# Optimization experiments

Hardware: AMD Instinct MI355X
Metric: run time of the kernel (lower is better)

Reference implementation:

```python
import jax, jax.numpy as jnp
import numpy as np

B, NQ, S, D = 8, 1024, 2048, 512

def setup_inputs() -> dict:
    key = jax.random.key(0)
    k1, k2, k3, k4 = jax.random.split(key, 4)
    queries = jax.random.normal(k1, (B, NQ, D), dtype=jnp.float32)
    keys = jax.random.normal(k2, (B, S, D), dtype=jnp.float32)
    values = jax.random.normal(k3, (B, S, D), dtype=jnp.float32)
    mask = jax.random.randint(k4, (B, NQ, S), 0, 2, dtype=jnp.int32)
    return {"queries": queries, "keys": keys, "values": values, "mask": mask}

def reference(queries, keys, values, mask):
    # scores: dot-product attention scores (b, nq, s)
    scores = jnp.einsum('bqd,bsd->bqs', queries, keys)
    attention_dist = jax.nn.softmax(scores, axis=2)
    # mask then renormalize over seq axis
    attention_dist = attention_dist * mask.astype(attention_dist.dtype)
    attention_dist = attention_dist / attention_dist.sum(axis=2, keepdims=True)
    # weighted sum of values: equivalent to (dist.unsqueeze(3) * values.unsqueeze(1)).sum(2)
    final_vector = jnp.einsum('bqs,bsd->bqd', attention_dist, values)
    return final_vector
```

## Files before the change

kernel.cpp:

```cpp
#include <hip/hip_runtime.h>


#define Bz 8
#define NQz 1024
#define Sz 2048
#define Dz 512
#define QTT 128
#define TS 32
#define KP 520
#define PP 40

typedef _Float16 f16x8 __attribute__((ext_vector_type(8)));
typedef float f32x4 __attribute__((ext_vector_type(4)));
typedef unsigned short ushort_t;

#define AS1(p) ((const __attribute__((address_space(1))) unsigned int*)(p))
#define AS3(p) ((__attribute__((address_space(3))) unsigned int*)(p))
#define DRAIN_ALL() __builtin_amdgcn_s_waitcnt(0)

__device__ __forceinline__ ushort_t f2h(float x) {
  _Float16 h = (_Float16)x;
  return __builtin_bit_cast(ushort_t, h);
}
__device__ __forceinline__ float h2f(ushort_t u) {
  return (float)__builtin_bit_cast(_Float16, u);
}

__global__ __launch_bounds__(256)
void prep(const float* __restrict__ K, const float* __restrict__ V,
          const int* __restrict__ Mi, ushort_t* __restrict__ Kf,
          ushort_t* __restrict__ Vt, unsigned* __restrict__ Mp) {
  __shared__ ushort_t sT[64][41];
  const int t = threadIdx.x;
  int bx = blockIdx.x;
  if (bx < 2048) {
    const size_t base = (size_t)bx * 4096 + t * 4;
#pragma unroll
    for (int i = 0; i < 4; ++i) {
      size_t e = base + i * 1024;
      float4 v = *(const float4*)(K + e);
      uint2 w;
      w.x = (unsigned)f2h(v.x) | ((unsigned)f2h(v.y) << 16);
      w.y = (unsigned)f2h(v.z) | ((unsigned)f2h(v.w) << 16);
      *(uint2*)(Kf + e) = w;
    }
    return;
  }
  bx -= 2048;
  if (bx < 4096) {
    const int b = bx >> 9;
    const int rest = bx & 511;
    const int st = rest >> 4;
    const int dt = rest & 15;
    const int s0 = st * 64, d0 = dt * 32;
    const float* Vb = V + ((size_t)b * Sz + s0) * Dz + d0;
#pragma unroll
    for (int i = 0; i < 2; ++i) {
      int idx = t + 256 * i;
      int s = idx >> 3;
      int dc = (idx & 7) * 4;
      float4 v = *(const float4*)(Vb + (size_t)s * Dz + dc);
      uint2 w;
      w.x = (unsigned)f2h(v.x) | ((unsigned)f2h(v.y) << 16);
      w.y = (unsigned)f2h(v.z) | ((unsigned)f2h(v.w) << 16);
      *(uint2*)(&sT[s][dc]) = w;
    }
    __syncthreads();
    ushort_t* VtB = Vt + ((size_t)b * Dz + d0) * Sz + s0;
    int d = t >> 3, c = t & 7;
    uint4 u;
    ushort_t* tp = (ushort_t*)&u;
#pragma unroll
    for (int j = 0; j < 8; ++j) tp[j] = sT[c * 8 + j][d];
    *(uint4*)(VtB + (size_t)d * Sz + c * 8) = u;
    return;
  }
  bx -= 4096;
  const int lane = t & 63;
#pragma unroll
  for (int i = 0; i < 4; ++i) {
    const size_t base = (size_t)bx * 4096 + i * 1024 + t * 4;
    const int4 mv = *(const int4*)(Mi + base);
    unsigned nib = (mv.x ? 1u : 0u) | (mv.y ? 2u : 0u) |
                   (mv.z ? 4u : 0u) | (mv.w ? 8u : 0u);
    unsigned v = nib << ((lane & 7) * 4);
    v |= __shfl_xor(v, 1);
    v |= __shfl_xor(v, 2);
    v |= __shfl_xor(v, 4);
    if ((lane & 7) == 0) Mp[bx * 128 + i * 32 + (t >> 3)] = v;
  }
}

template <int SPLIT>
__global__ __launch_bounds__(512, 2)
void attn_flash(const float* __restrict__ Q, const unsigned* __restrict__ Mp,
                const ushort_t* __restrict__ Kf, const ushort_t* __restrict__ Vt,
                ushort_t* __restrict__ Opart, float* __restrict__ Mpart,
                float* __restrict__ Lpart) {
  __shared__ ushort_t sK[2][TS][KP];
  __shared__ ushort_t sV[2][Dz][TS];
  __shared__ ushort_t sP[8][16][PP];

  const int tid  = threadIdx.x;
  const int wave = tid >> 6;
  const int lane = tid & 63;
  const int l16  = lane & 15;
  const int quad = lane >> 4;

  const int bxr = blockIdx.x;
  const int b   = bxr & 7;
  const int rest = bxr >> 3;
  const int qt  = rest / SPLIT;
  const int sh  = rest % SPLIT;
  const int q0  = qt * QTT;
  const int SLEN = Sz / SPLIT;
  const int NTt  = SLEN / TS;
  const int sbeg = sh * SLEN;
  const int qw   = q0 + wave * 16;

  const float*    Qb  = Q  + ((size_t)b * NQz + qw) * Dz;
  const ushort_t* KfB = Kf + (size_t)b * Sz * Dz;
  const ushort_t* VtB = Vt + (size_t)b * Dz * Sz;
  const unsigned* MpB = Mp + ((size_t)b * NQz + qw) * (Sz / 32);

  const int vql  = (lane & 3) ^ ((lane >> 3) & 3);
  const int vcol = (quad ^ ((l16 >> 1) & 3)) * 8;

  auto issue_tile = [&](int s0n, int bsel) {
#pragma unroll
    for (int j = 0; j < 4; ++j) {
      int row = wave * 4 + j;
      const ushort_t* gp = KfB + (size_t)(s0n + row) * Dz + lane * 8;
      __builtin_amdgcn_global_load_lds(AS1(gp), AS3(&sK[bsel][row][0]), 16, 0, 0);
    }
#pragma unroll
    for (int j = 0; j < 4; ++j) {
      int dbase = wave * 64 + j * 16;
      int d = dbase + (lane >> 2);
      const ushort_t* gp = VtB + (size_t)d * Sz + s0n + vql * 8;
      __builtin_amdgcn_global_load_lds(AS1(gp), AS3(&sV[bsel][dbase][0]), 16, 0, 0);
    }
  };
  auto load_mask = [&](int s0n) -> unsigned {
    return MpB[(size_t)l16 * (Sz / 32) + (s0n >> 5)];
  };

  issue_tile(sbeg, 0);
  unsigned msk_cur = load_mask(sbeg);

  f16x8 qa[16];
  {
    const float* qrow = Qb + (size_t)l16 * Dz;
#pragma unroll
    for (int kk = 0; kk < 16; ++kk) {
      const float4 a = *(const float4*)(qrow + kk * 32 + quad * 8);
      const float4 c = *(const float4*)(qrow + kk * 32 + quad * 8 + 4);
      f16x8 h;
      h[0] = (_Float16)a.x; h[1] = (_Float16)a.y;
      h[2] = (_Float16)a.z; h[3] = (_Float16)a.w;
      h[4] = (_Float16)c.x; h[5] = (_Float16)c.y;
      h[6] = (_Float16)c.z; h[7] = (_Float16)c.w;
      qa[kk] = h;
    }
  }
  if (NTt > 1) issue_tile(sbeg + TS, 1);
  DRAIN_ALL();
  __syncthreads();

  float m_ln = -1e30f, l_ln = 0.0f;
  f32x4 oacc[32];
#pragma unroll
  for (int nt = 0; nt < 32; ++nt) oacc[nt] = (f32x4){0.f, 0.f, 0.f, 0.f};

  const ushort_t* vbase0 = &sV[0][0][0] + (size_t)l16 * TS + vcol;
  const ushort_t* vbase1 = &sV[1][0][0] + (size_t)l16 * TS + vcol;

  for (int i = 0; i < NTt; ++i) {
    const int buf = i & 1;
    if (i) {
      DRAIN_ALL();
      __syncthreads();
      if (i + 1 < NTt) issue_tile(sbeg + (i + 1) * TS, buf ^ 1);
    }
    unsigned msk_nxt = (i + 1 < NTt) ? load_mask(sbeg + (i + 1) * TS) : 0u;

    f32x4 a00 = (f32x4){0.f,0.f,0.f,0.f}, a01 = (f32x4){0.f,0.f,0.f,0.f};
    f32x4 a10 = (f32x4){0.f,0.f,0.f,0.f}, a11 = (f32x4){0.f,0.f,0.f,0.f};
    {
      const ushort_t* kh0 = &sK[buf][l16][quad * 8];
      const ushort_t* kh1 = &sK[buf][16 + l16][quad * 8];
#pragma unroll
      for (int kk = 0; kk < 16; kk += 2) {
        f16x8 k00 = *(const f16x8*)(kh0 + kk * 32);
        f16x8 k10 = *(const f16x8*)(kh1 + kk * 32);
        f16x8 k01 = *(const f16x8*)(kh0 + kk * 32 + 32);
        f16x8 k11 = *(const f16x8*)(kh1 + kk * 32 + 32);
        a00 = __builtin_amdgcn_mfma_f32_16x16x32_f16(k00, qa[kk], a00, 0, 0, 0);
        a10 = __builtin_amdgcn_mfma_f32_16x16x32_f16(k10, qa[kk], a10, 0, 0, 0);
        a01 = __builtin_amdgcn_mfma_f32_16x16x32_f16(k01, qa[kk+1], a01, 0, 0, 0);
        a11 = __builtin_amdgcn_mfma_f32_16x16x32_f16(k11, qa[kk+1], a11, 0, 0, 0);
      }
    }
    f32x4 s0v, s1v;
#pragma unroll
    for (int r = 0; r < 4; ++r) { s0v[r] = a00[r] + a01[r]; s1v[r] = a10[r] + a11[r]; }

    const unsigned mb = msk_cur;
    float se0[4], se1[4];
#pragma unroll
    for (int r = 0; r < 4; ++r) {
      se0[r] = ((mb >> (quad * 4 + r)) & 1u)      ? s0v[r] : -1e30f;
      se1[r] = ((mb >> (16 + quad * 4 + r)) & 1u) ? s1v[r] : -1e30f;
    }
    float rmax = fmaxf(fmaxf(fmaxf(se0[0], se0[1]), fmaxf(se0[2], se0[3])),
                       fmaxf(fmaxf(se1[0], se1[1]), fmaxf(se1[2], se1[3])));
    rmax = fmaxf(rmax, __shfl_xor(rmax, 16));
    rmax = fmaxf(rmax, __shfl_xor(rmax, 32));

    ushort_t pb0[4], pb1[4];
    float rsum = 0.f;
#pragma unroll
    for (int r = 0; r < 4; ++r) {
      float p0 = ((mb >> (quad * 4 + r)) & 1u)      ? __expf(se0[r] - rmax) : 0.f;
      float p1 = ((mb >> (16 + quad * 4 + r)) & 1u) ? __expf(se1[r] - rmax) : 0.f;
      pb0[r] = f2h(p0); pb1[r] = f2h(p1);
      rsum += h2f(pb0[r]) + h2f(pb1[r]);
    }
    {
      uint2 w0, w1;
      w0.x = (unsigned)pb0[0] | ((unsigned)pb0[1] << 16);
      w0.y = (unsigned)pb0[2] | ((unsigned)pb0[3] << 16);
      w1.x = (unsigned)pb1[0] | ((unsigned)pb1[1] << 16);
      w1.y = (unsigned)pb1[2] | ((unsigned)pb1[3] << 16);
      *(uint2*)(&sP[wave][l16][quad * 4]) = w0;
      *(uint2*)(&sP[wave][l16][16 + quad * 4]) = w1;
    }
    rsum += __shfl_xor(rsum, 16);
    rsum += __shfl_xor(rsum, 32);

    float m_new = fmaxf(m_ln, rmax);
    float scl   = __expf(rmax - m_new);
    float al_ln = __expf(m_ln - m_new);
    bool  grw   = m_new > m_ln;
    l_ln = al_ln * l_ln + scl * rsum;
    m_ln = m_new;

    f16x8 praw = *(const f16x8*)(&sP[wave][l16][quad * 8]);
    f16x8 pa;
    {
      _Float16 sh16 = (_Float16)scl;
#pragma unroll
      for (int j = 0; j < 8; ++j) pa[j] = praw[j] * sh16;
    }

    if (__any((int)grw)) {
      float al[4];
#pragma unroll
      for (int r = 0; r < 4; ++r) al[r] = __shfl(al_ln, quad * 4 + r);
#pragma unroll
      for (int nt = 0; nt < 32; ++nt)
#pragma unroll
        for (int r = 0; r < 4; ++r) oacc[nt][r] *= al[r];
    }

    const ushort_t* vb_ = buf ? vbase1 : vbase0;
#pragma unroll
    for (int nt = 0; nt < 32; ++nt) {
      f16x8 vb = *(const f16x8*)(vb_ + nt * 512);
      oacc[nt] = __builtin_amdgcn_mfma_f32_16x16x32_f16(pa, vb, oacc[nt], 0, 0, 0);
    }

    msk_cur = msk_nxt;
  }

  const size_t rbase = (size_t)(b * SPLIT + sh) * NQz + q0 + wave * 16;
#pragma unroll
  for (int nt = 0; nt < 32; ++nt) {
#pragma unroll
    for (int r = 0; r < 4; ++r) {
      Opart[(rbase + quad * 4 + r) * Dz + nt * 16 + l16] = f2h(oacc[nt][r]);
    }
  }
  if (quad == 0) {
    Mpart[rbase + l16] = m_ln;
    Lpart[rbase + l16] = l_ln;
  }
}

template <int SPLIT>
__global__ __launch_bounds__(256)
void combine(const ushort_t* __restrict__ Opart, const float* __restrict__ Mpart,
             const float* __restrict__ Lpart, float* __restrict__ Out) {
  int gid = blockIdx.x * 256 + threadIdx.x;
  int row = gid >> 7;
  int b   = row >> 10;
  int q   = row & 1023;
  int c   = (gid & 127) * 4;
  float mv[SPLIT], lv[SPLIT];
  float m = -1e30f;
#pragma unroll
  for (int p = 0; p < SPLIT; ++p) {
    size_t ip = (size_t)(b * SPLIT + p) * NQz + q;
    mv[p] = Mpart[ip];
    lv[p] = Lpart[ip];
    m = fmaxf(m, mv[p]);
  }
  float w[SPLIT], denom = 0.f;
#pragma unroll
  for (int p = 0; p < SPLIT; ++p) {
    w[p] = __expf(mv[p] - m);
    denom += w[p] * lv[p];
  }
  float inv = 1.0f / denom;
  float4 o = {0.f, 0.f, 0.f, 0.f};
#pragma unroll
  for (int p = 0; p < SPLIT; ++p) {
    size_t ip = (size_t)(b * SPLIT + p) * NQz + q;
    const ushort_t* op = Opart + ip * Dz + c;
    uint2 raw = *(const uint2*)op;
    o.x += w[p] * h2f((ushort_t)(raw.x & 0xffff));
    o.y += w[p] * h2f((ushort_t)(raw.x >> 16));
    o.z += w[p] * h2f((ushort_t)(raw.y & 0xffff));
    o.w += w[p] * h2f((ushort_t)(raw.y >> 16));
  }
  o.x *= inv; o.y *= inv; o.z *= inv; o.w *= inv;
  *(float4*)(Out + ((size_t)b * NQz + q) * Dz + c) = o;
}

extern "C" void kernel_launch(void* const* d_in, const int* in_sizes, int n_in,
                              void* d_out, int out_size, void* d_ws, size_t ws_size,
                              hipStream_t stream) {
  const float* Q = (const float*)d_in[0];
  const float* K = (const float*)d_in[1];
  const float* V = (const float*)d_in[2];
  const int*   M = (const int*)d_in[3];
  float* O = (float*)d_out;

  const size_t NKV   = (size_t)Bz * Sz * Dz;
  const size_t maskW = (size_t)Bz * NQz * (Sz / 32);

  ushort_t* Kf = (ushort_t*)d_ws;
  ushort_t* Vt = Kf + NKV;
  unsigned* Mp = (unsigned*)(Vt + NKV);
  ushort_t* Opart = (ushort_t*)(Mp + maskW);

  auto need_bytes = [&](int S) -> size_t {
    return NKV * 2 * 2 + maskW * 4
         + (size_t)Bz * S * NQz * Dz * 2
         + (size_t)Bz * S * NQz * 4 * 2;
  };

  prep<<<dim3(10240), dim3(256), 0, stream>>>(K, V, M, Kf, Vt, Mp);

  if (ws_size >= need_bytes(4)) {
    constexpr int S = 4;
    float* Mpart = (float*)(Opart + (size_t)Bz * S * NQz * Dz);
    float* Lpart = Mpart + (size_t)Bz * S * NQz;
    attn_flash<S><<<dim3(8 * (NQz / QTT) * S), dim3(512), 0, stream>>>(
        Q, Mp, Kf, Vt, Opart, Mpart, Lpart);
    combine<S><<<dim3(4096), dim3(256), 0, stream>>>(Opart, Mpart, Lpart, O);
  } else {
    constexpr int S = 2;
    float* Mpart = (float*)(Opart + (size_t)Bz * S * NQz * Dz);
    float* Lpart = Mpart + (size_t)Bz * S * NQz;
    attn_flash<S><<<dim3(8 * (NQz / QTT) * S), dim3(512), 0, stream>>>(
        Q, Mp, Kf, Vt, Opart, Mpart, Lpart);
    combine<S><<<dim3(4096), dim3(256), 0, stream>>>(Opart, Mpart, Lpart, O);
  }
}
```

Measured before the change: 246.9 us.

## Partition PV by D columns per wave, load V directly into registers

```diff
diff --git a/kernel.cpp b/kernel.cpp
--- a/kernel.cpp
+++ b/kernel.cpp
@@ -98,8 +98,8 @@
                 ushort_t* __restrict__ Opart, float* __restrict__ Mpart,
                 float* __restrict__ Lpart) {
   __shared__ ushort_t sK[2][TS][KP];
-  __shared__ ushort_t sV[2][Dz][TS];
-  __shared__ ushort_t sP[8][16][PP];
+  __shared__ ushort_t sP[QTT][PP];
+  __shared__ float    sAl[QTT];
 
   const int tid  = threadIdx.x;
   const int wave = tid >> 6;
@@ -123,29 +123,21 @@
   const ushort_t* VtB = Vt + (size_t)b * Dz * Sz;
   const unsigned* MpB = Mp + ((size_t)b * NQz + qw) * (Sz / 32);
 
-  const int vql  = (lane & 3) ^ ((lane >> 3) & 3);
-  const int vcol = (quad ^ ((l16 >> 1) & 3)) * 8;
-
-  auto issue_tile = [&](int s0n, int bsel) {
+  auto issue_k = [&](int s0n, int bsel) {
 #pragma unroll
     for (int j = 0; j < 4; ++j) {
       int row = wave * 4 + j;
       const ushort_t* gp = KfB + (size_t)(s0n + row) * Dz + lane * 8;
       __builtin_amdgcn_global_load_lds(AS1(gp), AS3(&sK[bsel][row][0]), 16, 0, 0);
     }
-#pragma unroll
-    for (int j = 0; j < 4; ++j) {
-      int dbase = wave * 64 + j * 16;
-      int d = dbase + (lane >> 2);
-      const ushort_t* gp = VtB + (size_t)d * Sz + s0n + vql * 8;
-      __builtin_amdgcn_global_load_lds(AS1(gp), AS3(&sV[bsel][dbase][0]), 16, 0, 0);
-    }
   };
   auto load_mask = [&](int s0n) -> unsigned {
     return MpB[(size_t)l16 * (Sz / 32) + (s0n >> 5)];
   };
-
-  issue_tile(sbeg, 0);
+  const ushort_t* VtW = VtB + (size_t)(wave * 64 + l16) * Sz;
+
+  issue_k(sbeg, 0);
+  if (NTt > 1) issue_k(sbeg + TS, 1);
   unsigned msk_cur = load_mask(sbeg);
 
   f16x8 qa[16];
@@ -163,7 +155,6 @@
       qa[kk] = h;
     }
   }
-  if (NTt > 1) issue_tile(sbeg + TS, 1);
   DRAIN_ALL();
   __syncthreads();
 
@@ -172,17 +163,15 @@
 #pragma unroll
   for (int nt = 0; nt < 32; ++nt) oacc[nt] = (f32x4){0.f, 0.f, 0.f, 0.f};
 
-  const ushort_t* vbase0 = &sV[0][0][0] + (size_t)l16 * TS + vcol;
-  const ushort_t* vbase1 = &sV[1][0][0] + (size_t)l16 * TS + vcol;
-
   for (int i = 0; i < NTt; ++i) {
     const int buf = i & 1;
-    if (i) {
-      DRAIN_ALL();
-      __syncthreads();
-      if (i + 1 < NTt) issue_tile(sbeg + (i + 1) * TS, buf ^ 1);
-    }
-    unsigned msk_nxt = (i + 1 < NTt) ? load_mask(sbeg + (i + 1) * TS) : 0u;
+    const int s0  = sbeg + i * TS;
+
+    f16x8 vb[4];
+#pragma unroll
+    for (int dt = 0; dt < 4; ++dt)
+      vb[dt] = *(const f16x8*)(VtW + (size_t)(dt * 16) * Sz + s0 + quad * 8);
+    unsigned msk_nxt = (i + 1 < NTt) ? load_mask(s0 + TS) : 0u;
 
     f32x4 a00 = (f32x4){0.f,0.f,0.f,0.f}, a01 = (f32x4){0.f,0.f,0.f,0.f};
     f32x4 a10 = (f32x4){0.f,0.f,0.f,0.f}, a11 = (f32x4){0.f,0.f,0.f,0.f};
@@ -217,12 +206,15 @@
     rmax = fmaxf(rmax, __shfl_xor(rmax, 16));
     rmax = fmaxf(rmax, __shfl_xor(rmax, 32));
 
+    float m_new = fmaxf(m_ln, rmax);
+    float al_ln = __expf(m_ln - m_new);
+
     ushort_t pb0[4], pb1[4];
     float rsum = 0.f;
 #pragma unroll
     for (int r = 0; r < 4; ++r) {
-      float p0 = ((mb >> (quad * 4 + r)) & 1u)      ? __expf(se0[r] - rmax) : 0.f;
-      float p1 = ((mb >> (16 + quad * 4 + r)) & 1u) ? __expf(se1[r] - rmax) : 0.f;
+      float p0 = ((mb >> (quad * 4 + r)) & 1u)      ? __expf(se0[r] - m_new) : 0.f;
+      float p1 = ((mb >> (16 + quad * 4 + r)) & 1u) ? __expf(se1[r] - m_new) : 0.f;
       pb0[r] = f2h(p0); pb1[r] = f2h(p1);
       rsum += h2f(pb0[r]) + h2f(pb1[r]);
     }
@@ -232,58 +224,59 @@
       w0.y = (unsigned)pb0[2] | ((unsigned)pb0[3] << 16);
       w1.x = (unsigned)pb1[0] | ((unsigned)pb1[1] << 16);
       w1.y = (unsigned)pb1[2] | ((unsigned)pb1[3] << 16);
-      *(uint2*)(&sP[wave][l16][quad * 4]) = w0;
-      *(uint2*)(&sP[wave][l16][16 + quad * 4]) = w1;
-    }
+      *(uint2*)(&sP[wave * 16 + l16][quad * 4]) = w0;
+      *(uint2*)(&sP[wave * 16 + l16][16 + quad * 4]) = w1;
+    }
+    if (quad == 0) sAl[wave * 16 + l16] = al_ln;
     rsum += __shfl_xor(rsum, 16);
     rsum += __shfl_xor(rsum, 32);
-
-    float m_new = fmaxf(m_ln, rmax);
-    float scl   = __expf(rmax - m_new);
-    float al_ln = __expf(m_ln - m_new);
-    bool  grw   = m_new > m_ln;
-    l_ln = al_ln * l_ln + scl * rsum;
+    l_ln = al_ln * l_ln + rsum;
     m_ln = m_new;
 
-    f16x8 praw = *(const f16x8*)(&sP[wave][l16][quad * 8]);
-    f16x8 pa;
-    {
-      _Float16 sh16 = (_Float16)scl;
-#pragma unroll
-      for (int j = 0; j < 8; ++j) pa[j] = praw[j] * sh16;
-    }
-
-    if (__any((int)grw)) {
-      float al[4];
-#pragma unroll
-      for (int r = 0; r < 4; ++r) al[r] = __shfl(al_ln, quad * 4 + r);
-#pragma unroll
-      for (int nt = 0; nt < 32; ++nt)
-#pragma unroll
-        for (int r = 0; r < 4; ++r) oacc[nt][r] *= al[r];
-    }
-
-    const ushort_t* vb_ = buf ? vbase1 : vbase0;
-#pragma unroll
-    for (int nt = 0; nt < 32; ++nt) {
-      f16x8 vb = *(const f16x8*)(vb_ + nt * 512);
-      oacc[nt] = __builtin_amdgcn_mfma_f32_16x16x32_f16(pa, vb, oacc[nt], 0, 0, 0);
+    asm volatile("s_waitcnt vmcnt(5)" ::: "memory");
+    asm volatile("s_waitcnt lgkmcnt(0)" ::: "memory");
+    __builtin_amdgcn_s_barrier();
+    asm volatile("" ::: "memory");
+
+    if (i + 2 < NTt) issue_k(sbeg + (i + 2) * TS, buf);
+
+#pragma unroll
+    for (int qb = 0; qb < 8; ++qb) {
+      f32x4 alr = *(const f32x4*)(&sAl[qb * 16 + quad * 4]);
+#pragma unroll
+      for (int dt = 0; dt < 4; ++dt)
+#pragma unroll
+        for (int r = 0; r < 4; ++r) oacc[qb * 4 + dt][r] *= alr[r];
+    }
+
+#pragma unroll
+    for (int qb = 0; qb < 8; ++qb) {
+      f16x8 pa = *(const f16x8*)(&sP[qb * 16 + l16][quad * 8]);
+#pragma unroll
+      for (int dt = 0; dt < 4; ++dt) {
+        oacc[qb * 4 + dt] = __builtin_amdgcn_mfma_f32_16x16x32_f16(
+            pa, vb[dt], oacc[qb * 4 + dt], 0, 0, 0);
+      }
     }
 
     msk_cur = msk_nxt;
   }
 
-  const size_t rbase = (size_t)(b * SPLIT + sh) * NQz + q0 + wave * 16;
-#pragma unroll
-  for (int nt = 0; nt < 32; ++nt) {
-#pragma unroll
-    for (int r = 0; r < 4; ++r) {
-      Opart[(rbase + quad * 4 + r) * Dz + nt * 16 + l16] = f2h(oacc[nt][r]);
+  const size_t rbase = (size_t)(b * SPLIT + sh) * NQz + q0;
+#pragma unroll
+  for (int qb = 0; qb < 8; ++qb) {
+#pragma unroll
+    for (int dt = 0; dt < 4; ++dt) {
+#pragma unroll
+      for (int r = 0; r < 4; ++r) {
+        Opart[(rbase + qb * 16 + quad * 4 + r) * Dz + wave * 64 + dt * 16 + l16] =
+            f2h(oacc[qb * 4 + dt][r]);
+      }
     }
   }
   if (quad == 0) {
-    Mpart[rbase + l16] = m_ln;
-    Lpart[rbase + l16] = l_ln;
+    Mpart[rbase + wave * 16 + l16] = m_ln;
+    Lpart[rbase + wave * 16 + l16] = l_ln;
   }
 }
 
```

Result: no change. 247.6 us (+0.3%).

## Fuse split-KV combine into attention kernel via last-block atomic counter

Applied to the files above, without the earlier changes.

```diff
diff --git a/kernel.cpp b/kernel.cpp
--- a/kernel.cpp
+++ b/kernel.cpp
@@ -29,11 +29,13 @@
 __global__ __launch_bounds__(256)
 void prep(const float* __restrict__ K, const float* __restrict__ V,
           const int* __restrict__ Mi, ushort_t* __restrict__ Kf,
-          ushort_t* __restrict__ Vt, unsigned* __restrict__ Mp) {
+          ushort_t* __restrict__ Vt, unsigned* __restrict__ Mp,
+          int* __restrict__ Cnt) {
   __shared__ ushort_t sT[64][41];
   const int t = threadIdx.x;
   int bx = blockIdx.x;
   if (bx < 2048) {
+    if (bx == 0 && t < 64) Cnt[t] = 0;
     const size_t base = (size_t)bx * 4096 + t * 4;
 #pragma unroll
     for (int i = 0; i < 4; ++i) {
@@ -96,7 +98,8 @@
 void attn_flash(const float* __restrict__ Q, const unsigned* __restrict__ Mp,
                 const ushort_t* __restrict__ Kf, const ushort_t* __restrict__ Vt,
                 ushort_t* __restrict__ Opart, float* __restrict__ Mpart,
-                float* __restrict__ Lpart) {
+                float* __restrict__ Lpart, int* __restrict__ Cnt,
+                float* __restrict__ Out) {
   __shared__ ushort_t sK[2][TS][KP];
   __shared__ ushort_t sV[2][Dz][TS];
   __shared__ ushort_t sP[8][16][PP];
@@ -285,46 +288,53 @@
     Mpart[rbase + l16] = m_ln;
     Lpart[rbase + l16] = l_ln;
   }
-}
-
-template <int SPLIT>
-__global__ __launch_bounds__(256)
-void combine(const ushort_t* __restrict__ Opart, const float* __restrict__ Mpart,
-             const float* __restrict__ Lpart, float* __restrict__ Out) {
-  int gid = blockIdx.x * 256 + threadIdx.x;
-  int row = gid >> 7;
-  int b   = row >> 10;
-  int q   = row & 1023;
-  int c   = (gid & 127) * 4;
-  float mv[SPLIT], lv[SPLIT];
-  float m = -1e30f;
-#pragma unroll
-  for (int p = 0; p < SPLIT; ++p) {
-    size_t ip = (size_t)(b * SPLIT + p) * NQz + q;
-    mv[p] = Mpart[ip];
-    lv[p] = Lpart[ip];
-    m = fmaxf(m, mv[p]);
-  }
-  float w[SPLIT], denom = 0.f;
-#pragma unroll
-  for (int p = 0; p < SPLIT; ++p) {
-    w[p] = __expf(mv[p] - m);
-    denom += w[p] * lv[p];
-  }
-  float inv = 1.0f / denom;
-  float4 o = {0.f, 0.f, 0.f, 0.f};
-#pragma unroll
-  for (int p = 0; p < SPLIT; ++p) {
-    size_t ip = (size_t)(b * SPLIT + p) * NQz + q;
-    const ushort_t* op = Opart + ip * Dz + c;
-    uint2 raw = *(const uint2*)op;
-    o.x += w[p] * h2f((ushort_t)(raw.x & 0xffff));
-    o.y += w[p] * h2f((ushort_t)(raw.x >> 16));
-    o.z += w[p] * h2f((ushort_t)(raw.y & 0xffff));
-    o.w += w[p] * h2f((ushort_t)(raw.y >> 16));
-  }
-  o.x *= inv; o.y *= inv; o.z *= inv; o.w *= inv;
-  *(float4*)(Out + ((size_t)b * NQz + q) * Dz + c) = o;
+
+  __threadfence();
+  __shared__ int sLast;
+  __syncthreads();
+  if (tid == 0) sLast = atomicAdd(&Cnt[b * 8 + qt], 1);
+  __syncthreads();
+  if (sLast == SPLIT - 1) {
+    __threadfence();
+    __shared__ float sW[SPLIT][QTT];
+    __shared__ float sInv[QTT];
+    for (int rr = tid; rr < QTT; rr += 512) {
+      float mv[SPLIT], lv[SPLIT], mmax = -1e30f;
+#pragma unroll
+      for (int p = 0; p < SPLIT; ++p) {
+        size_t ip = (size_t)(b * SPLIT + p) * NQz + q0 + rr;
+        mv[p] = Mpart[ip]; lv[p] = Lpart[ip];
+        mmax = fmaxf(mmax, mv[p]);
+      }
+      float den = 0.f;
+#pragma unroll
+      for (int p = 0; p < SPLIT; ++p) {
+        float w = __expf(mv[p] - mmax);
+        sW[p][rr] = w;
+        den += w * lv[p];
+      }
+      sInv[rr] = 1.0f / den;
+    }
+    __syncthreads();
+    const int col = tid & 127;
+    const int rg  = tid >> 7;
+    for (int rr = rg * 32; rr < rg * 32 + 32; ++rr) {
+      float inv = sInv[rr];
+      float4 acc = {0.f, 0.f, 0.f, 0.f};
+#pragma unroll
+      for (int p = 0; p < SPLIT; ++p) {
+        size_t ip = ((size_t)(b * SPLIT + p) * NQz + q0 + rr) * Dz + col * 4;
+        uint2 raw = *(const uint2*)(Opart + ip);
+        float w = sW[p][rr];
+        acc.x += w * h2f((ushort_t)(raw.x & 0xffff));
+        acc.y += w * h2f((ushort_t)(raw.x >> 16));
+        acc.z += w * h2f((ushort_t)(raw.y & 0xffff));
+        acc.w += w * h2f((ushort_t)(raw.y >> 16));
+      }
+      acc.x *= inv; acc.y *= inv; acc.z *= inv; acc.w *= inv;
+      *(float4*)(Out + ((size_t)b * NQz + q0 + rr) * Dz + col * 4) = acc;
+    }
+  }
 }
 
 extern "C" void kernel_launch(void* const* d_in, const int* in_sizes, int n_in,
@@ -342,29 +352,28 @@
   ushort_t* Kf = (ushort_t*)d_ws;
   ushort_t* Vt = Kf + NKV;
   unsigned* Mp = (unsigned*)(Vt + NKV);
-  ushort_t* Opart = (ushort_t*)(Mp + maskW);
+  int* Cnt = (int*)(Mp + maskW);
+  ushort_t* Opart = (ushort_t*)(Cnt + 64);
 
   auto need_bytes = [&](int S) -> size_t {
-    return NKV * 2 * 2 + maskW * 4
+    return NKV * 2 * 2 + maskW * 4 + 256
          + (size_t)Bz * S * NQz * Dz * 2
          + (size_t)Bz * S * NQz * 4 * 2;
   };
 
-  prep<<<dim3(10240), dim3(256), 0, stream>>>(K, V, M, Kf, Vt, Mp);
+  prep<<<dim3(10240), dim3(256), 0, stream>>>(K, V, M, Kf, Vt, Mp, Cnt);
 
   if (ws_size >= need_bytes(4)) {
     constexpr int S = 4;
     float* Mpart = (float*)(Opart + (size_t)Bz * S * NQz * Dz);
     float* Lpart = Mpart + (size_t)Bz * S * NQz;
     attn_flash<S><<<dim3(8 * (NQz / QTT) * S), dim3(512), 0, stream>>>(
-        Q, Mp, Kf, Vt, Opart, Mpart, Lpart);
-    combine<S><<<dim3(4096), dim3(256), 0, stream>>>(Opart, Mpart, Lpart, O);
+        Q, Mp, Kf, Vt, Opart, Mpart, Lpart, Cnt, O);
   } else {
     constexpr int S = 2;
     float* Mpart = (float*)(Opart + (size_t)Bz * S * NQz * Dz);
     float* Lpart = Mpart + (size_t)Bz * S * NQz;
     attn_flash<S><<<dim3(8 * (NQz / QTT) * S), dim3(512), 0, stream>>>(
-        Q, Mp, Kf, Vt, Opart, Mpart, Lpart);
-    combine<S><<<dim3(4096), dim3(256), 0, stream>>>(Opart, Mpart, Lpart, O);
-  }
-}
+        Q, Mp, Kf, Vt, Opart, Mpart, Lpart, Cnt, O);
+  }
+}
```

New measurement: 354.5 us. 43.6% more time.
